# Kernel optimization log

Measured on AMD Instinct MI355X. Metric: run time of the kernel, lower is better.

## Reference

```python
import jax, jax.numpy as jnp
import numpy as np

# Dimensions (match init_kwargs / input_specs)
B, N, E, H, L, FF = 32, 512, 1024, 8, 3, 2048
KD = E // H          # key_dim = val_dim = 128 (projection width of W_query/W_key/W_val)
DK = KD // H         # 16 = actual per-head dim after the raw (H,B,N,-1) view
NORM = 1.0 / np.sqrt(KD)  # module uses 1/sqrt(key_dim)
MASK_FILL = -30.0    # evaluate=False path


def setup_inputs() -> dict:
    key = jax.random.key(0)
    ks = jax.random.split(key, 11)
    f32 = jnp.float32
    x = jax.random.normal(ks[0], (B * N, E), f32)
    mask = jax.random.randint(ks[1], (B, N), 0, 2).astype(bool)
    # Stacked per-layer params; torch init: uniform(-1/sqrt(fan_in), 1/sqrt(fan_in))
    def u(k, shape, fan):
        s = 1.0 / np.sqrt(fan)
        return jax.random.uniform(k, shape, f32, -s, s)
    Wq = u(ks[2], (L, KD, E), E)
    Wk = u(ks[3], (L, KD, E), E)
    Wv = u(ks[4], (L, KD, E), E)
    Wo = u(ks[5], (L, E, KD), KD)
    bo = u(ks[6], (L, E), E)
    W1 = u(ks[7], (L, FF, E), E)
    b1 = u(ks[8], (L, FF), FF)
    W2 = u(ks[9], (L, E, FF), FF)
    b2 = u(ks[10], (L, E), E)
    return {"x": x, "mask": mask, "Wq": Wq, "Wk": Wk, "Wv": Wv,
            "Wo": Wo, "bo": bo, "W1": W1, "b1": b1, "W2": W2, "b2": b2}


def _mha(h, Wq, Wk, Wv, Wo, bo, mask):
    # h: (B*N, E). Raw row-major view (torch .view == jnp.reshape) into (H,B,N,DK),
    # which mixes token/feature axes exactly as the original module does.
    Q = (h @ Wq.T).reshape(H, B, N, DK)
    K = (h @ Wk.T).reshape(H, B, N, DK)
    V = (h @ Wv.T).reshape(H, B, N, DK)
    compat = NORM * jnp.einsum('hbnd,hbmd->hbnm', Q, K)  # (H,B,N,N)
    m = mask[None, :, None, :]                            # mask key positions
    compat = jnp.where(m, MASK_FILL, compat)
    attn = jax.nn.softmax(compat, axis=-1)
    attn = jnp.where(m, 0.0, attn)                        # re-zero masked entries
    heads = jnp.einsum('hbnm,hbmd->hbnd', attn, V)        # (H,B,N,DK)
    out = heads.transpose(1, 2, 0, 3).reshape(B * N, H * DK) @ Wo.T + bo
    return out


def reference(x, mask, Wq, Wk, Wv, Wo, bo, W1, b1, W2, b2):
    h = x
    for l in range(L):
        h = h + _mha(h, Wq[l], Wk[l], Wv[l], Wo[l], bo[l], mask)
        h = h + (jax.nn.relu(h @ W1[l].T + b1[l]) @ W2[l].T + b2[l])
    return h, h.reshape(B, N, E).mean(axis=1)
```

## Files before the change

kernel.cpp:

```cpp
#include <hip/hip_runtime.h>
#include <stdint.h>


typedef __attribute__((ext_vector_type(8))) short short8;
typedef __attribute__((ext_vector_type(4))) float floatx4;

#define NORM_ 0.08838834764831845f

__device__ __forceinline__ float bf2f(unsigned short u) {
    union { unsigned int i; float f; } x; x.i = ((unsigned int)u) << 16; return x.f;
}
__device__ __forceinline__ unsigned short f2bf(float f) {
    union { float f; unsigned int i; } x; x.f = f;
    unsigned int u = x.i;
    u += 0x7FFFu + ((u >> 16) & 1u);
    return (unsigned short)(u >> 16);
}
__device__ __forceinline__ void async_cp16(const void* g, void* l) {
    __builtin_amdgcn_global_load_lds((const __attribute__((address_space(1))) void*)g,
                                     (__attribute__((address_space(3))) void*)l, 16, 0, 0);
}

__global__ __launch_bounds__(256) void detect_dtype(const unsigned int* __restrict__ x,
                                                    int* __restrict__ flag)
{
    __shared__ int good, bad;
    if (threadIdx.x == 0) { good = 0; bad = 0; }
    __syncthreads();
    int g = 0, b = 0;
    for (int i = threadIdx.x; i < 4096; i += 256) {
        unsigned int lo = x[i] & 0xFFFFu;
        if (lo != 0u) {
            unsigned int e = (lo >> 7) & 0xFFu;
            if (e >= 90u && e <= 145u) ++g; else ++b;
        }
    }
    atomicAdd(&good, g); atomicAdd(&bad, b);
    __syncthreads();
    if (threadIdx.x == 0) *flag = (bad > good) ? 1 : 0;
}

__global__ __launch_bounds__(256) void conv_to_bf16(const void* __restrict__ src,
                                                    unsigned short* __restrict__ dst,
                                                    int n, const int* __restrict__ flag)
{
    const int i = (blockIdx.x * 256 + threadIdx.x) * 8;
    if (i >= n) return;
    if (*flag) {
        const float* s = (const float*)src + i;
        floatx4 a = *(const floatx4*)s;
        floatx4 b = *(const floatx4*)(s + 4);
        short8 o;
        o[0] = (short)f2bf(a[0]); o[1] = (short)f2bf(a[1]);
        o[2] = (short)f2bf(a[2]); o[3] = (short)f2bf(a[3]);
        o[4] = (short)f2bf(b[0]); o[5] = (short)f2bf(b[1]);
        o[6] = (short)f2bf(b[2]); o[7] = (short)f2bf(b[3]);
        *(short8*)(dst + i) = o;
    } else {
        *(short8*)(dst + i) = *(const short8*)((const unsigned short*)src + i);
    }
}

__global__ __launch_bounds__(256) void init_h(const void* __restrict__ x,
                                              float* __restrict__ hf,
                                              unsigned short* __restrict__ hb,
                                              const int* __restrict__ flag)
{
    const size_t i = ((size_t)blockIdx.x * 256 + threadIdx.x) * 8;
    if (*flag) {
        const float* s = (const float*)x + i;
        floatx4 a = *(const floatx4*)s;
        floatx4 b = *(const floatx4*)(s + 4);
        short8 o;
        o[0] = (short)f2bf(a[0]); o[1] = (short)f2bf(a[1]);
        o[2] = (short)f2bf(a[2]); o[3] = (short)f2bf(a[3]);
        o[4] = (short)f2bf(b[0]); o[5] = (short)f2bf(b[1]);
        o[6] = (short)f2bf(b[2]); o[7] = (short)f2bf(b[3]);
        *(short8*)(hb + i) = o;
        *(floatx4*)(hf + i) = a;
        *(floatx4*)(hf + i + 4) = b;
    } else {
        short8 v = *(const short8*)((const unsigned short*)x + i);
        *(short8*)(hb + i) = v;
        #pragma unroll
        for (int e = 0; e < 8; ++e) hf[i + e] = bf2f((unsigned short)v[e]);
    }
}

__global__ __launch_bounds__(256) void mask_expand(const unsigned int* __restrict__ mraw,
                                                   float* __restrict__ maskf)
{
    __shared__ unsigned int r[4];
    if (threadIdx.x < 4) r[threadIdx.x] = 0;
    __syncthreads();
    unsigned int gt1 = 0, badb = 0, badh = 0, lo3f = 0;
    for (int i = threadIdx.x; i < 4096; i += 256) {
        unsigned int w = mraw[i];
        if (w > 1u) gt1 = 1;
        if (w & 0xFEFEFEFEu) badb = 1;
        unsigned int lo = w & 0xFFFFu, hi = w >> 16;
        if ((lo != 0u && lo != 0x3F80u) || (hi != 0u && hi != 0x3F80u)) badh = 1;
        if (lo == 0x3F80u) lo3f = 1;
    }
    if (gt1) atomicOr(&r[0], 1u);
    if (badb) atomicOr(&r[1], 1u);
    if (badh) atomicOr(&r[2], 1u);
    if (lo3f) atomicOr(&r[3], 1u);
    __syncthreads();
    int cls;
    if (!r[0]) cls = 0;
    else if (!r[1]) cls = 1;
    else if (!r[2]) cls = r[3] ? 2 : 3;
    else cls = 0;

    const int gid = blockIdx.x * 256 + threadIdx.x;
    bool m;
    if (cls == 0)      m = ((const int*)mraw)[gid] != 0;
    else if (cls == 1) m = ((const unsigned char*)mraw)[gid] != 0;
    else if (cls == 2) m = ((const unsigned short*)mraw)[gid] != 0;
    else               m = mraw[gid] != 0u;
    maskf[gid] = m ? 1.0f : 0.0f;
}

enum { EPI_NONE = 0, EPI_BIAS_RELU = 1, EPI_BIAS_RES = 2 };

template<int EPI>
__global__ __launch_bounds__(256) void gemm_bt(
    const unsigned short* __restrict__ A,
    const unsigned short* __restrict__ Bq,
    const unsigned short* __restrict__ Bk,
    const unsigned short* __restrict__ Bv,
    unsigned short* __restrict__ Cq,
    unsigned short* __restrict__ Ck,
    unsigned short* __restrict__ Cv,
    const unsigned short* __restrict__ bias,
    float* __restrict__ hf,
    unsigned short* __restrict__ hb,
    int N, int K)
{
    __shared__ __align__(16) unsigned short As[128 * 32];
    __shared__ __align__(16) unsigned short Bs[128 * 32];

    const int t = threadIdx.x;
    const int lane = t & 63;
    const int wave = t >> 6;
    const int bm = blockIdx.x;
    const int bn = blockIdx.y;
    const int bz = blockIdx.z;

    const unsigned short* Bmat = (bz == 0) ? Bq : ((bz == 1) ? Bk : Bv);
    unsigned short* C = (bz == 0) ? Cq : ((bz == 1) ? Ck : Cv);

    const int wm = (wave >> 1) * 64;
    const int wn = (wave & 1) * 64;

    const int srow = t >> 2;
    const int scol = (t & 3) * 8;
    const unsigned short* Ag = A + (size_t)(bm * 128 + srow) * K + scol;
    const unsigned short* Bg = Bmat + (size_t)(bn * 128 + srow) * K + scol;
    unsigned short* As0 = &As[srow * 32 + scol];
    unsigned short* As1 = &As[(srow + 64) * 32 + scol];
    unsigned short* Bs0 = &Bs[srow * 32 + scol];
    unsigned short* Bs1 = &Bs[(srow + 64) * 32 + scol];
    const size_t rstep = (size_t)64 * K;

    const int fl = lane & 15;
    const int fk = (lane >> 4) * 8;
    int aoff[4], boff[4];
    #pragma unroll
    for (int i = 0; i < 4; ++i) {
        aoff[i] = (wm + i * 16 + fl) * 32 + fk;
        boff[i] = (wn + i * 16 + fl) * 32 + fk;
    }

    floatx4 acc[4][4];
    #pragma unroll
    for (int i = 0; i < 4; ++i)
        #pragma unroll
        for (int j = 0; j < 4; ++j) {
            acc[i][j][0] = 0.f; acc[i][j][1] = 0.f;
            acc[i][j][2] = 0.f; acc[i][j][3] = 0.f;
        }

    for (int k0 = 0; k0 < K; k0 += 32) {
        __syncthreads();
        async_cp16(Ag + k0, As0);
        async_cp16(Ag + k0 + rstep, As1);
        async_cp16(Bg + k0, Bs0);
        async_cp16(Bg + k0 + rstep, Bs1);
        __syncthreads();

        short8 af[4], bfr[4];
        #pragma unroll
        for (int i = 0; i < 4; ++i) af[i] = *(const short8*)&As[aoff[i]];
        #pragma unroll
        for (int j = 0; j < 4; ++j) bfr[j] = *(const short8*)&Bs[boff[j]];
        #pragma unroll
        for (int i = 0; i < 4; ++i)
            #pragma unroll
            for (int j = 0; j < 4; ++j)
                acc[i][j] = __builtin_amdgcn_mfma_f32_16x16x32_bf16(af[i], bfr[j], acc[i][j], 0, 0, 0);
    }

    const int r0 = (lane >> 4) * 4;
    #pragma unroll
    for (int j = 0; j < 4; ++j) {
        const int gcol = bn * 128 + wn + j * 16 + fl;
        float bval = 0.f;
        if (EPI != EPI_NONE) bval = bf2f(bias[gcol]);
        #pragma unroll
        for (int i = 0; i < 4; ++i) {
            const int growb = bm * 128 + wm + i * 16 + r0;
            #pragma unroll
            for (int r = 0; r < 4; ++r) {
                const size_t idx = (size_t)(growb + r) * N + gcol;
                float v = acc[i][j][r];
                if (EPI == EPI_NONE) {
                    C[idx] = f2bf(v);
                } else if (EPI == EPI_BIAS_RELU) {
                    v += bval;
                    v = v > 0.f ? v : 0.f;
                    C[idx] = f2bf(v);
                } else {
                    float nh = hf[idx] + v + bval;
                    hf[idx] = nh;
                    hb[idx] = f2bf(nh);
                }
            }
        }
    }
}

__global__ __launch_bounds__(128) void attn_mfma(
    const unsigned short* __restrict__ Q,
    const unsigned short* __restrict__ Kx,
    const unsigned short* __restrict__ Vx,
    const float* __restrict__ maskf,
    unsigned short* __restrict__ Out)
{
    __shared__ __align__(16) unsigned short Vt[16 * 520];
    __shared__ __align__(16) unsigned short Pb[2][64 * 40];
    __shared__ float Ms[512];
    __shared__ float cnt_s;

    const int t = threadIdx.x;
    const int lane = t & 63;
    const int wave = t >> 6;
    const int p = blockIdx.x >> 2;
    const int qq = blockIdx.x & 3;
    const int b2 = p & 31;
    const int h2 = p >> 5;
    const int fm = lane & 15;
    const int g = lane >> 4;

    const unsigned short* Qg = Q + (size_t)p * 8192;
    const unsigned short* Kg = Kx + (size_t)p * 8192;
    const unsigned short* Vg = Vx + (size_t)p * 8192;

    #pragma unroll
    for (int rr = 0; rr < 4; ++rr) {
        const int row = t * 4 + rr;
        short8 v0 = *(const short8*)&Vg[row * 16];
        short8 v1 = *(const short8*)&Vg[row * 16 + 8];
        #pragma unroll
        for (int d = 0; d < 8; ++d) Vt[d * 520 + row] = (unsigned short)v0[d];
        #pragma unroll
        for (int d = 0; d < 8; ++d) Vt[(d + 8) * 520 + row] = (unsigned short)v1[d];
    }
    if (t == 0) cnt_s = 0.f;
    __syncthreads();
    float pc = 0.f;
    #pragma unroll
    for (int it = 0; it < 4; ++it) {
        int i = it * 128 + t;
        float mv = maskf[b2 * 512 + i];
        Ms[i] = mv; pc += mv;
    }
    atomicAdd(&cnt_s, pc);
    __syncthreads();
    const float cnt = cnt_s;

    const int qbase = qq * 128 + wave * 64;
    short8 qf[4];
    #pragma unroll
    for (int i = 0; i < 4; ++i) {
        short8 z = {0,0,0,0,0,0,0,0};
        if (g < 2) z = *(const short8*)&Qg[(qbase + i * 16 + fm) * 16 + g * 8];
        qf[i] = z;
    }

    float m_[4][4], l_[4][4];
    floatx4 O[4];
    #pragma unroll
    for (int i = 0; i < 4; ++i) {
        #pragma unroll
        for (int r = 0; r < 4; ++r) { m_[i][r] = -1e30f; l_[i][r] = 0.f; }
        O[i][0] = 0.f; O[i][1] = 0.f; O[i][2] = 0.f; O[i][3] = 0.f;
    }

    unsigned short* Pw = &Pb[wave][0];

    for (int kb = 0; kb < 512; kb += 32) {
        short8 kf0 = {0,0,0,0,0,0,0,0}, kf1 = {0,0,0,0,0,0,0,0};
        if (g < 2) {
            kf0 = *(const short8*)&Kg[(kb + fm) * 16 + g * 8];
            kf1 = *(const short8*)&Kg[(kb + 16 + fm) * 16 + g * 8];
        }
        const float msk0 = Ms[kb + fm];
        const float msk1 = Ms[kb + 16 + fm];

        floatx4 zero4 = {0.f, 0.f, 0.f, 0.f};
        floatx4 s0[4], s1[4];
        #pragma unroll
        for (int i = 0; i < 4; ++i) {
            s0[i] = __builtin_amdgcn_mfma_f32_16x16x32_bf16(qf[i], kf0, zero4, 0, 0, 0);
            s1[i] = __builtin_amdgcn_mfma_f32_16x16x32_bf16(qf[i], kf1, zero4, 0, 0, 0);
        }

        #pragma unroll
        for (int i = 0; i < 4; ++i) {
            #pragma unroll
            for (int r = 0; r < 4; ++r) {
                float a0 = (msk0 != 0.f) ? -1e30f : s0[i][r] * NORM_;
                float a1 = (msk1 != 0.f) ? -1e30f : s1[i][r] * NORM_;
                float mx = fmaxf(a0, a1);
                mx = fmaxf(mx, __shfl_xor(mx, 1));
                mx = fmaxf(mx, __shfl_xor(mx, 2));
                mx = fmaxf(mx, __shfl_xor(mx, 4));
                mx = fmaxf(mx, __shfl_xor(mx, 8));
                const float mo = m_[i][r];
                const float mn = fmaxf(mo, mx);
                const float alpha = __expf(mo - mn);
                float w0 = (msk0 != 0.f) ? 0.f : __expf(a0 - mn);
                float w1 = (msk1 != 0.f) ? 0.f : __expf(a1 - mn);
                float rs = w0 + w1;
                rs += __shfl_xor(rs, 1);
                rs += __shfl_xor(rs, 2);
                rs += __shfl_xor(rs, 4);
                rs += __shfl_xor(rs, 8);
                l_[i][r] = l_[i][r] * alpha + rs;
                m_[i][r] = mn;
                O[i][r] *= alpha;
                const int qloc = i * 16 + g * 4 + r;
                Pw[qloc * 40 + fm] = f2bf(w0);
                Pw[qloc * 40 + 16 + fm] = f2bf(w1);
            }
        }
        asm volatile("s_waitcnt lgkmcnt(0)" ::: "memory");

        short8 vtf = *(const short8*)&Vt[fm * 520 + kb + g * 8];
        #pragma unroll
        for (int i = 0; i < 4; ++i) {
            short8 pf = *(const short8*)&Pw[(i * 16 + fm) * 40 + g * 8];
            O[i] = __builtin_amdgcn_mfma_f32_16x16x32_bf16(pf, vtf, O[i], 0, 0, 0);
        }
    }

    #pragma unroll
    for (int i = 0; i < 4; ++i) {
        #pragma unroll
        for (int r = 0; r < 4; ++r) {
            const float M = fmaxf(m_[i][r], -30.f);
            const float adj = __expf(m_[i][r] - M);
            const float lf = l_[i][r] * adj + cnt * __expf(-30.f - M);
            const float oval = O[i][r] * adj / lf;
            const int n = qbase + i * 16 + g * 4 + r;
            Out[((size_t)(b2 * 512 + n)) * 128 + h2 * 16 + fm] = f2bf(oval);
        }
    }
}

__global__ __launch_bounds__(256) void write_h(const float* __restrict__ hf,
                                               void* __restrict__ out,
                                               const int* __restrict__ flag)
{
    const size_t i = ((size_t)blockIdx.x * 256 + threadIdx.x) * 4;
    floatx4 v = *(const floatx4*)&hf[i];
    if (*flag) {
        *(floatx4*)((float*)out + i) = v;
    } else {
        unsigned int p0 = (unsigned int)f2bf(v[0]) | ((unsigned int)f2bf(v[1]) << 16);
        unsigned int p1 = (unsigned int)f2bf(v[2]) | ((unsigned int)f2bf(v[3]) << 16);
        unsigned int* o = (unsigned int*)((unsigned short*)out + i);
        o[0] = p0; o[1] = p1;
    }
}

__global__ __launch_bounds__(256) void mean_kernel(const float* __restrict__ hf,
                                                   void* __restrict__ out,
                                                   const int* __restrict__ flag)
{
    const int b = blockIdx.x >> 2;
    const int e = ((blockIdx.x & 3) * 256) + threadIdx.x;
    float s = 0.f;
    for (int n = 0; n < 512; ++n) s += hf[((size_t)(b * 512 + n)) * 1024 + e];
    s *= (1.0f / 512.0f);
    const size_t off = (size_t)16384 * 1024 + b * 1024 + e;
    if (*flag) ((float*)out)[off] = s;
    else       ((unsigned short*)out)[off] = f2bf(s);
}

extern "C" void kernel_launch(void* const* d_in, const int* in_sizes, int n_in,
                              void* d_out, int out_size, void* d_ws, size_t ws_size,
                              hipStream_t stream)
{
    const void* x  = d_in[0];
    const unsigned int* mask = (const unsigned int*)d_in[1];

    char* ws = (char*)d_ws;
    float* hf = (float*)ws;                     ws += (size_t)16384 * 1024 * 4;
    unsigned short* hb = (unsigned short*)ws;   ws += (size_t)16384 * 1024 * 2;
    char* shared_rg = ws;                       ws += (size_t)16384 * 2048 * 2;
    unsigned short* act = (unsigned short*)shared_rg;
    unsigned short* q  = (unsigned short*)shared_rg;
    unsigned short* k  = q + (size_t)16384 * 128;
    unsigned short* v  = k + (size_t)16384 * 128;
    unsigned short* ao = v + (size_t)16384 * 128;
    unsigned short* cWq = (unsigned short*)ws;  ws += (size_t)393216 * 2;
    unsigned short* cWk = (unsigned short*)ws;  ws += (size_t)393216 * 2;
    unsigned short* cWv = (unsigned short*)ws;  ws += (size_t)393216 * 2;
    unsigned short* cWo = (unsigned short*)ws;  ws += (size_t)393216 * 2;
    unsigned short* cbo = (unsigned short*)ws;  ws += (size_t)3072 * 2;
    unsigned short* cW1 = (unsigned short*)ws;  ws += (size_t)6291456 * 2;
    unsigned short* cb1 = (unsigned short*)ws;  ws += (size_t)6144 * 2;
    unsigned short* cW2 = (unsigned short*)ws;  ws += (size_t)6291456 * 2;
    unsigned short* cb2 = (unsigned short*)ws;  ws += (size_t)3072 * 2;
    float* maskf = (float*)ws;                  ws += (size_t)16384 * 4;
    int* flag = (int*)ws;                       ws += 256;

    detect_dtype<<<1, 256, 0, stream>>>((const unsigned int*)x, flag);

    auto conv = [&](const void* s, unsigned short* d, int n) {
        conv_to_bf16<<<(n / 8 + 255) / 256, 256, 0, stream>>>(s, d, n, flag);
    };
    conv(d_in[2], cWq, 393216);
    conv(d_in[3], cWk, 393216);
    conv(d_in[4], cWv, 393216);
    conv(d_in[5], cWo, 393216);
    conv(d_in[6], cbo, 3072);
    conv(d_in[7], cW1, 6291456);
    conv(d_in[8], cb1, 6144);
    conv(d_in[9], cW2, 6291456);
    conv(d_in[10], cb2, 3072);

    mask_expand<<<64, 256, 0, stream>>>(mask, maskf);
    init_h<<<8192, 256, 0, stream>>>(x, hf, hb, flag);

    for (int l = 0; l < 3; ++l) {
        const unsigned short* wq  = cWq + (size_t)l * 131072;
        const unsigned short* wk  = cWk + (size_t)l * 131072;
        const unsigned short* wv  = cWv + (size_t)l * 131072;
        const unsigned short* wo  = cWo + (size_t)l * 131072;
        const unsigned short* bol = cbo + (size_t)l * 1024;
        const unsigned short* w1  = cW1 + (size_t)l * 2097152;
        const unsigned short* b1l = cb1 + (size_t)l * 2048;
        const unsigned short* w2  = cW2 + (size_t)l * 2097152;
        const unsigned short* b2l = cb2 + (size_t)l * 1024;

        gemm_bt<EPI_NONE><<<dim3(128, 1, 3), 256, 0, stream>>>(
            hb, wq, wk, wv, q, k, v, nullptr, nullptr, nullptr, 128, 1024);
        attn_mfma<<<1024, 128, 0, stream>>>(q, k, v, maskf, ao);
        gemm_bt<EPI_BIAS_RES><<<dim3(128, 8, 1), 256, 0, stream>>>(
            ao, wo, wo, wo, nullptr, nullptr, nullptr, bol, hf, hb, 1024, 128);
        gemm_bt<EPI_BIAS_RELU><<<dim3(128, 16, 1), 256, 0, stream>>>(
            hb, w1, w1, w1, act, act, act, b1l, nullptr, nullptr, 2048, 1024);
        gemm_bt<EPI_BIAS_RES><<<dim3(128, 8, 1), 256, 0, stream>>>(
            act, w2, w2, w2, nullptr, nullptr, nullptr, b2l, hf, hb, 1024, 2048);
    }

    write_h<<<16384, 256, 0, stream>>>(hf, d_out, flag);
    mean_kernel<<<128, 256, 0, stream>>>(hf, d_out, flag);
}
```

Measured before the change: 1.362 ms.

## Double-buffer GEMM LDS tiles with BK=64 and XOR swizzle

Rewrites the GEMM main loop to use two LDS buffers with a K-tile of 64, so the async global-to-LDS loads for the next tile are issued before the current tile's MFMAs run. An XOR swizzle on the LDS column index is added to reduce bank conflicts on the fragment reads. Synchronisation moves from __syncthreads to explicit vmcnt waits and s_barrier. This targets load latency and barrier stalls, at the cost of four times the LDS per block (64 KB), which may reduce occupancy.

```diff
diff --git a/kernel.cpp b/kernel.cpp
--- a/kernel.cpp
+++ b/kernel.cpp
@@ -138,8 +138,9 @@
     unsigned short* __restrict__ hb,
     int N, int K)
 {
-    __shared__ __align__(16) unsigned short As[128 * 32];
-    __shared__ __align__(16) unsigned short Bs[128 * 32];
+    constexpr int BK = 64;
+    __shared__ __align__(16) unsigned short As[2][128 * BK];
+    __shared__ __align__(16) unsigned short Bs[2][128 * BK];
 
     const int t = threadIdx.x;
     const int lane = t & 63;
@@ -154,23 +155,22 @@
     const int wm = (wave >> 1) * 64;
     const int wn = (wave & 1) * 64;
 
-    const int srow = t >> 2;
-    const int scol = (t & 3) * 8;
+    const int srow = t >> 3;
+    const int scol = (((t & 7) ^ ((t >> 3) & 7)) * 8);
     const unsigned short* Ag = A + (size_t)(bm * 128 + srow) * K + scol;
     const unsigned short* Bg = Bmat + (size_t)(bn * 128 + srow) * K + scol;
-    unsigned short* As0 = &As[srow * 32 + scol];
-    unsigned short* As1 = &As[(srow + 64) * 32 + scol];
-    unsigned short* Bs0 = &Bs[srow * 32 + scol];
-    unsigned short* Bs1 = &Bs[(srow + 64) * 32 + scol];
-    const size_t rstep = (size_t)64 * K;
+    const size_t gstep = (size_t)32 * K;
 
     const int fl = lane & 15;
-    const int fk = (lane >> 4) * 8;
+    const int g = lane >> 4;
+    const int s7 = fl & 7;
+    const int swz0 = (g ^ s7) * 8;
+    const int swz1 = ((g + 4) ^ s7) * 8;
     int aoff[4], boff[4];
     #pragma unroll
     for (int i = 0; i < 4; ++i) {
-        aoff[i] = (wm + i * 16 + fl) * 32 + fk;
-        boff[i] = (wn + i * 16 + fl) * 32 + fk;
+        aoff[i] = (wm + i * 16 + fl) * BK;
+        boff[i] = (wn + i * 16 + fl) * BK;
     }
 
     floatx4 acc[4][4];
@@ -182,24 +182,46 @@
             acc[i][j][2] = 0.f; acc[i][j][3] = 0.f;
         }
 
-    for (int k0 = 0; k0 < K; k0 += 32) {
-        __syncthreads();
-        async_cp16(Ag + k0, As0);
-        async_cp16(Ag + k0 + rstep, As1);
-        async_cp16(Bg + k0, Bs0);
-        async_cp16(Bg + k0 + rstep, Bs1);
-        __syncthreads();
-
-        short8 af[4], bfr[4];
-        #pragma unroll
-        for (int i = 0; i < 4; ++i) af[i] = *(const short8*)&As[aoff[i]];
-        #pragma unroll
-        for (int j = 0; j < 4; ++j) bfr[j] = *(const short8*)&Bs[boff[j]];
-        #pragma unroll
-        for (int i = 0; i < 4; ++i)
-            #pragma unroll
-            for (int j = 0; j < 4; ++j)
-                acc[i][j] = __builtin_amdgcn_mfma_f32_16x16x32_bf16(af[i], bfr[j], acc[i][j], 0, 0, 0);
+    const int NT = K / BK;
+
+    #pragma unroll
+    for (int r = 0; r < 4; ++r) {
+        async_cp16(Ag + r * gstep, &As[0][t * 8 + r * 2048]);
+        async_cp16(Bg + r * gstep, &Bs[0][t * 8 + r * 2048]);
+    }
+
+    for (int it = 0; it < NT; ++it) {
+        const int cur = it & 1;
+        if (it + 1 < NT) {
+            const int nxt = cur ^ 1;
+            const size_t koff = (size_t)(it + 1) * BK;
+            #pragma unroll
+            for (int r = 0; r < 4; ++r) {
+                async_cp16(Ag + koff + r * gstep, &As[nxt][t * 8 + r * 2048]);
+                async_cp16(Bg + koff + r * gstep, &Bs[nxt][t * 8 + r * 2048]);
+            }
+            asm volatile("s_waitcnt vmcnt(8)" ::: "memory");
+        } else {
+            asm volatile("s_waitcnt vmcnt(0)" ::: "memory");
+        }
+        asm volatile("s_barrier" ::: "memory");
+
+        #pragma unroll
+        for (int ks = 0; ks < 2; ++ks) {
+            const int sw = ks ? swz1 : swz0;
+            short8 af[4], bfr[4];
+            #pragma unroll
+            for (int i = 0; i < 4; ++i) af[i] = *(const short8*)&As[cur][aoff[i] + sw];
+            #pragma unroll
+            for (int j = 0; j < 4; ++j) bfr[j] = *(const short8*)&Bs[cur][boff[j] + sw];
+            #pragma unroll
+            for (int i = 0; i < 4; ++i)
+                #pragma unroll
+                for (int j = 0; j < 4; ++j)
+                    acc[i][j] = __builtin_amdgcn_mfma_f32_16x16x32_bf16(af[i], bfr[j], acc[i][j], 0, 0, 0);
+        }
+        if (it + 1 < NT)
+            asm volatile("s_barrier" ::: "memory");
     }
 
     const int r0 = (lane >> 4) * 4;
```

Measured after the change: 1.237 ms. 1.1x faster.
